# Kernel tuning notes

Measured on AMD Instinct MI355X. Metric: run time of the kernel, lower is better.

The kernel has to match this reference:

```python
import jax, jax.numpy as jnp
import numpy as np

# dims matching init_kwargs / input_specs
N, C, H, W = 8, 256, 64, 64
OUT_C, KH, KW = 256, 3, 3
STRIDE, PAD = 1, 1
OUT_H = (H - KH + 2 * PAD) // STRIDE + 1  # 64
OUT_W = (W - KW + 2 * PAD) // STRIDE + 1  # 64
K = KH * KW


def setup_inputs() -> dict:
    key = jax.random.key(0)
    k1, k2, k3 = jax.random.split(key, 3)
    x = jax.random.normal(k1, (N, C, H, W), dtype=jnp.float32)
    offset = jax.random.normal(k2, (N, 2 * K, OUT_H, OUT_W), dtype=jnp.float32)
    # kaiming-uniform-ish scale for weight (fan_in = C*KH*KW)
    bound = 1.0 / np.sqrt(C * KH * KW)
    weight = jax.random.uniform(k3, (OUT_C, C, KH, KW), dtype=jnp.float32,
                                minval=-bound, maxval=bound)
    return {"input": x, "offset": offset, "weight": weight}


def _deform_conv(x, offset, weight):
    # base sampling positions in pixel coords: y = oy*stride + ky - pad
    ky = jnp.repeat(jnp.arange(KH, dtype=jnp.float32) - PAD, KW)  # [K]
    kx = jnp.tile(jnp.arange(KW, dtype=jnp.float32) - PAD, KH)    # [K]
    oy = jnp.arange(OUT_H, dtype=jnp.float32) * STRIDE            # [outH]
    ox = jnp.arange(OUT_W, dtype=jnp.float32) * STRIDE            # [outW]
    base_y = ky[:, None, None] + oy[None, :, None]  # [K, outH, 1]
    base_x = kx[:, None, None] + ox[None, None, :]  # [K, 1, outW]

    off = offset.reshape(N, K, 2, OUT_H, OUT_W)
    y = base_y[None] + off[:, :, 0]  # [N, K, outH, outW], offset channel 0 = dy
    xp = base_x[None] + off[:, :, 1]  # channel 1 = dx

    # bilinear sample with zero padding (grid_sample align_corners=True, zeros)
    y0 = jnp.floor(y)
    x0 = jnp.floor(xp)
    bidx = jnp.arange(N)[:, None, None, None]
    acc = jnp.zeros((N, K, OUT_H, OUT_W, C), dtype=x.dtype)
    for dy in (0.0, 1.0):
        for dx in (0.0, 1.0):
            yi = y0 + dy
            xi = x0 + dx
            wgt = (1.0 - jnp.abs(y - yi)) * (1.0 - jnp.abs(xp - xi))
            valid = ((yi >= 0) & (yi <= H - 1) & (xi >= 0) & (xi <= W - 1))
            yc = jnp.clip(yi, 0, H - 1).astype(jnp.int32)
            xc = jnp.clip(xi, 0, W - 1).astype(jnp.int32)
            g = x[bidx, :, yc, xc]  # [N, K, outH, outW, C]
            acc = acc + g * (wgt * valid.astype(x.dtype))[..., None]

    # weight.view(outC, -1) flattens (C, KH, KW) -> (C, K) ordering
    w = weight.reshape(OUT_C, C, K)
    out = jnp.einsum('nkhwc,ock->nohw', acc, w)  # [N, outC, outH, outW]
    return out


def reference(input, offset, weight):
    # NOTE: original forward never adds bias -> faithfully omitted
    return _deform_conv(input, offset, weight)
```

## Files before the change

kernel.cpp:

```cpp
#include <hip/hip_runtime.h>
#include <hip/hip_fp16.h>
#include <stdint.h>


typedef _Float16 half8 __attribute__((ext_vector_type(8)));
typedef float f32x4 __attribute__((ext_vector_type(4)));

__device__ __forceinline__ __half2 h2(uint32_t u) {
  return __builtin_bit_cast(__half2, u);
}
__device__ __forceinline__ uint32_t packh2f(float a, float b) {
  return __builtin_bit_cast(uint32_t, __floats2half2_rn(a, b));
}
__device__ __forceinline__ __half2 duplo(uint32_t u) {
  return __half2half2(__builtin_bit_cast(__half, (unsigned short)(u & 0xffffu)));
}
__device__ __forceinline__ __half2 duphi(uint32_t u) {
  return __half2half2(__builtin_bit_cast(__half, (unsigned short)(u >> 16)));
}

__global__ __launch_bounds__(256) void prep_all_kernel(
    const float* __restrict__ x, const float* __restrict__ w,
    const float* __restrict__ offset,
    unsigned short* __restrict__ xb, unsigned short* __restrict__ w3s,
    unsigned short* __restrict__ coords) {
  __shared__ float tile[64][65];
  int tid = threadIdx.x;
  if (blockIdx.x < 2048) {
    int bn   = blockIdx.x >> 8;
    int rem  = blockIdx.x & 255;
    int y    = rem >> 2;
    int cblk = rem & 3;
    const float* src = x + ((size_t)(bn * 256 + cblk * 64)) * 4096 + y * 64;
#pragma unroll
    for (int i = 0; i < 4; ++i) {
      int u  = i * 256 + tid;
      int cl = u >> 4;
      int xs = (u & 15) * 4;
      float4 v = *(const float4*)(src + cl * 4096 + xs);
      tile[cl][xs] = v.x; tile[cl][xs + 1] = v.y;
      tile[cl][xs + 2] = v.z; tile[cl][xs + 3] = v.w;
    }
    __syncthreads();
    unsigned short* dst = xb + ((size_t)(bn * 64 + y) * 64) * 256 + cblk * 64;
#pragma unroll
    for (int i = 0; i < 8; ++i) {
      int v2  = i * 256 + tid;
      int xc  = v2 >> 5;
      int cl2 = (v2 & 31) * 2;
      *(uint32_t*)(dst + xc * 256 + cl2) = packh2f(tile[cl2][xc], tile[cl2 + 1][xc]);
    }
  } else if (blockIdx.x < 4352) {
    int idx = (blockIdx.x - 2048) * 256 + tid;
    int t    = idx >> 14;
    int r2   = idx & 16383;
    int e    = r2 & 7;
    int lane = (r2 >> 3) & 63;
    int ks   = (r2 >> 9) & 1;
    int nn   = (r2 >> 10) & 3;
    int wcol = (r2 >> 12) & 3;
    int oc = wcol * 64 + nn * 16 + (lane & 15);
    int kk = (ks * 4 + (lane >> 4)) * 8 + e;
    int c  = (t & 3) * 64 + kk;
    int k  = t >> 2;
    w3s[idx] = __builtin_bit_cast(unsigned short, __float2half(w[(oc * 256 + c) * 9 + k]));
  } else {
    int idx = (blockIdx.x - 4352) * 256 + tid;
    int ow  = idx & 63;
    int oh  = (idx >> 6) & 63;
    int r   = idx >> 12;
    int k   = r % 9;
    int bn  = r / 9;
    int ky = k / 3 - 1;
    int kx = k % 3 - 1;
    float offy = offset[((bn * 18 + 2 * k    ) * 64 + oh) * 64 + ow];
    float offx = offset[((bn * 18 + 2 * k + 1) * 64 + oh) * 64 + ow];
    float y = (float)(oh + ky) + offy;
    float x2 = (float)(ow + kx) + offx;
    float y0f = floorf(y), x0f = floorf(x2);
    float fy = y - y0f, fx = x2 - x0f;
    int y0 = (int)y0f, x0 = (int)x0f;
    int y1 = y0 + 1, x1 = x0 + 1;
    float vy0 = (y0 >= 0 && y0 <= 63) ? 1.0f : 0.0f;
    float vy1 = (y1 >= 0 && y1 <= 63) ? 1.0f : 0.0f;
    float vx0 = (x0 >= 0 && x0 <= 63) ? 1.0f : 0.0f;
    float vx1 = (x1 >= 0 && x1 <= 63) ? 1.0f : 0.0f;
    float wy0 = (1.0f - fy) * vy0, wy1 = fy * vy1;
    float wx0 = (1.0f - fx) * vx0, wx1 = fx * vx1;
    int y0c = min(max(y0, 0), 63), y1c = min(max(y1, 0), 63);
    int x0c = min(max(x0, 0), 63), x1c = min(max(x1, 0), 63);
    unsigned short ent[8];
    ent[0] = __builtin_bit_cast(unsigned short, __float2half(wy0 * wx0));
    ent[1] = __builtin_bit_cast(unsigned short, __float2half(wy0 * wx1));
    ent[2] = __builtin_bit_cast(unsigned short, __float2half(wy1 * wx0));
    ent[3] = __builtin_bit_cast(unsigned short, __float2half(wy1 * wx1));
    ent[4] = (unsigned short)(y0c * 64 + x0c);
    ent[5] = (unsigned short)(y0c * 64 + x1c);
    ent[6] = (unsigned short)(y1c * 64 + x0c);
    ent[7] = (unsigned short)(y1c * 64 + x1c);
    *(uint4*)(coords + (size_t)idx * 8) = *(const uint4*)ent;
  }
}

__global__ __launch_bounds__(512, 4) void deform_mfma_kernel(
    const unsigned short* __restrict__ xb,
    const unsigned short* __restrict__ coords,
    const unsigned short* __restrict__ w3s,
    float* __restrict__ out) {
  __shared__ __align__(16) unsigned short At[2][64 * 64];
  __shared__ __align__(16) unsigned short Bt[2][16384];

  int bn  = blockIdx.x & 7;
  int oh  = blockIdx.x >> 3;
  int tid = threadIdx.x;

  int w    = tid >> 6;
  int lane = tid & 63;
  int wrow = w & 1;
  int wcol = w >> 1;
  int mrow = lane & 15;
  int quad = lane >> 4;

  int srow = tid >> 3;
  int sg   = tid & 7;

  const char* xbc = (const char*)(xb + (size_t)bn * (64 * 64 * 256));
  const unsigned short* cb = coords + ((size_t)((bn * 9) * 64 + oh) * 64 + srow) * 8;

  int aw0  = srow * 64 + ((sg ^ (srow & 7)) * 8);
  int grp0 = quad ^ (mrow & 7);
  int grp1 = (4 + quad) ^ (mrow & 7);
  int a_base = (wrow * 32 + mrow) * 64;
  int b_off  = wcol * 4096 + lane * 8;
  int d_off  = w * 2048 + lane * 8;

  f32x4 acc[2][4] = {};

  __half2 w00, w01, w02, w03;
  uint32_t o00, o01, o02, o03;
  uint4 cn;
  uint4 ga0, ga1, ga2, ga3;

#define EBAR()                                                                  \
  {                                                                             \
    asm volatile("s_waitcnt vmcnt(0) lgkmcnt(0)" ::: "memory");                 \
    __builtin_amdgcn_sched_barrier(0);                                          \
    __builtin_amdgcn_s_barrier();                                               \
    asm volatile("" ::: "memory");                                              \
  }
#define CBAR()                                                                  \
  {                                                                             \
    asm volatile("s_waitcnt lgkmcnt(0)" ::: "memory");                          \
    __builtin_amdgcn_s_barrier();                                               \
    asm volatile("" ::: "memory");                                              \
  }
#define VMW(N)                                                                  \
  {                                                                             \
    asm volatile("s_waitcnt vmcnt(" #N ")" ::: "memory");                       \
    __builtin_amdgcn_sched_barrier(0);                                          \
  }

#define BDMA(TT, BB)                                                            \
  {                                                                             \
    const unsigned short* src = w3s + (size_t)(TT) * 16384 + d_off;             \
    unsigned short* dst = &Bt[BB][0] + w * 2048;                                \
    _Pragma("unroll")                                                           \
    for (int j = 0; j < 4; ++j) {                                               \
      __builtin_amdgcn_global_load_lds(                                         \
          (const __attribute__((address_space(1))) void*)(src + j * 512),       \
          (__attribute__((address_space(3))) void*)(dst + j * 512),             \
          16, 0, 0);                                                            \
    }                                                                           \
  }

#define TAPSETUP_R(CE)                                                          \
  {                                                                             \
    w00 = duplo((CE).x); w01 = duphi((CE).x);                                   \
    w02 = duplo((CE).y); w03 = duphi((CE).y);                                   \
    o00 = (((CE).z & 0xffffu) << 9) + sg * 16;                                  \
    o01 = (((CE).z >> 16) << 9) + sg * 16;                                      \
    o02 = (((CE).w & 0xffffu) << 9) + sg * 16;                                  \
    o03 = (((CE).w >> 16) << 9) + sg * 16;                                      \
  }

#define AGATHER(TT)                                                             \
  {                                                                             \
    ga0 = *(const uint4*)(xbc + o00 + ((TT) & 3) * 128);                        \
    ga1 = *(const uint4*)(xbc + o01 + ((TT) & 3) * 128);                        \
    ga2 = *(const uint4*)(xbc + o02 + ((TT) & 3) * 128);                        \
    ga3 = *(const uint4*)(xbc + o03 + ((TT) & 3) * 128);                        \
  }

#define AMATH(ATP)                                                              \
  {                                                                             \
    VMW(4)                                                                      \
    __half2 r0 = __hmul2(h2(ga0.x), w00);                                       \
    r0 = __hfma2(h2(ga1.x), w01, r0); r0 = __hfma2(h2(ga2.x), w02, r0);         \
    r0 = __hfma2(h2(ga3.x), w03, r0);                                           \
    __half2 r1 = __hmul2(h2(ga0.y), w00);                                       \
    r1 = __hfma2(h2(ga1.y), w01, r1); r1 = __hfma2(h2(ga2.y), w02, r1);         \
    r1 = __hfma2(h2(ga3.y), w03, r1);                                           \
    __half2 r2 = __hmul2(h2(ga0.z), w00);                                       \
    r2 = __hfma2(h2(ga1.z), w01, r2); r2 = __hfma2(h2(ga2.z), w02, r2);         \
    r2 = __hfma2(h2(ga3.z), w03, r2);                                           \
    __half2 r3 = __hmul2(h2(ga0.w), w00);                                       \
    r3 = __hfma2(h2(ga1.w), w01, r3); r3 = __hfma2(h2(ga2.w), w02, r3);         \
    r3 = __hfma2(h2(ga3.w), w03, r3);                                           \
    uint4 pk;                                                                   \
    pk.x = __builtin_bit_cast(uint32_t, r0);                                    \
    pk.y = __builtin_bit_cast(uint32_t, r1);                                    \
    pk.z = __builtin_bit_cast(uint32_t, r2);                                    \
    pk.w = __builtin_bit_cast(uint32_t, r3);                                    \
    *(uint4*)((ATP) + aw0) = pk;                                                \
  }

#define COMPUTE(ATP, BTP)                                                       \
  {                                                                             \
    half8 bfr[2][4];                                                            \
    _Pragma("unroll")                                                           \
    for (int nn = 0; nn < 4; ++nn) {                                            \
      bfr[0][nn] = *(const half8*)((BTP) + b_off + (nn * 2 + 0) * 512);         \
      bfr[1][nn] = *(const half8*)((BTP) + b_off + (nn * 2 + 1) * 512);         \
    }                                                                           \
    __builtin_amdgcn_s_setprio(1);                                              \
    _Pragma("unroll")                                                           \
    for (int m = 0; m < 2; ++m) {                                               \
      half8 af0 = *(const half8*)((ATP) + a_base + m * 1024 + grp0 * 8);        \
      half8 af1 = *(const half8*)((ATP) + a_base + m * 1024 + grp1 * 8);        \
      _Pragma("unroll")                                                         \
      for (int nn = 0; nn < 4; ++nn) {                                          \
        acc[m][nn] = __builtin_amdgcn_mfma_f32_16x16x32_f16(af0, bfr[0][nn], acc[m][nn], 0, 0, 0); \
        acc[m][nn] = __builtin_amdgcn_mfma_f32_16x16x32_f16(af1, bfr[1][nn], acc[m][nn], 0, 0, 0); \
      }                                                                         \
    }                                                                           \
    __builtin_amdgcn_s_setprio(0);                                              \
  }

  {
    uint4 ce0 = *(const uint4*)cb;
    AGATHER(0)
    TAPSETUP_R(ce0)
  }
  AGATHER(0)
  BDMA(0, 0)
  AMATH(&At[0][0])
  CBAR()

  for (int tap = 0; tap < 9; ++tap) {
#pragma unroll
    for (int cc = 0; cc < 4; ++cc) {
      const int t = tap * 4 + cc;
      EBAR()
      if (t < 35) {
        if (cc == 3) TAPSETUP_R(cn)
        if (cc == 2 && tap < 8) cn = *(const uint4*)(cb + (tap + 1) * 32768);
        AGATHER(t + 1)
        if (cc & 1) { BDMA(t + 1, 0) } else { BDMA(t + 1, 1) }
      }
      if (cc & 1) { COMPUTE(&At[1][0], &Bt[1][0]) } else { COMPUTE(&At[0][0], &Bt[0][0]) }
      if (t < 35) {
        if (cc & 1) { AMATH(&At[0][0]) } else { AMATH(&At[1][0]) }
      }
      CBAR()
    }
  }

  float* outp = out + (size_t)bn * 256 * 4096 + (size_t)oh * 64;
#pragma unroll
  for (int m = 0; m < 2; ++m) {
    int ow0 = wrow * 32 + m * 16 + quad * 4;
#pragma unroll
    for (int nn = 0; nn < 4; ++nn) {
      int oc = wcol * 64 + nn * 16 + mrow;
      *(f32x4*)(outp + (size_t)oc * 4096 + ow0) = acc[m][nn];
    }
  }
#undef EBAR
#undef CBAR
#undef VMW
#undef BDMA
#undef TAPSETUP_R
#undef AGATHER
#undef AMATH
#undef COMPUTE
}

extern "C" void kernel_launch(void* const* d_in, const int* in_sizes, int n_in,
                              void* d_out, int out_size, void* d_ws, size_t ws_size,
                              hipStream_t stream) {
  (void)in_sizes; (void)n_in; (void)out_size; (void)ws_size;
  const float* x      = (const float*)d_in[0];
  const float* offset = (const float*)d_in[1];
  const float* weight = (const float*)d_in[2];
  float* out = (float*)d_out;

  unsigned short* xb     = (unsigned short*)d_ws;
  unsigned short* w3s    = xb + (size_t)8 * 64 * 64 * 256;
  unsigned short* coords = w3s + (size_t)36 * 16384;

  prep_all_kernel<<<5504, 256, 0, stream>>>(x, weight, offset, xb, w3s, coords);
  deform_mfma_kernel<<<512, 512, 0, stream>>>(xb, coords, w3s, out);
}
```

Before: 144.1 us.

## Halve block to four waves, each computing 64x64 output tile

The MFMA kernel now runs 256 threads (4 waves) per block instead of 512. Each wave covers all 64 output columns for its 64 output channels, so the per-wave accumulator grows from 2x4 to 4x4 tiles. Each thread gathers and bilinearly blends two 16-byte chunks per tap and issues twice the weight DMA. The vmcnt waits are adjusted to match the larger number of outstanding loads. The aim is more MFMA work per A/B fragment load and less barrier cost per unit of work, at the price of more registers per thread, lower occupancy, and fewer waves available to hide gather latency.

```diff
diff --git a/kernel.cpp b/kernel.cpp
--- a/kernel.cpp
+++ b/kernel.cpp
@@ -102,7 +102,7 @@
   }
 }
 
-__global__ __launch_bounds__(512, 4) void deform_mfma_kernel(
+__global__ __launch_bounds__(256, 2) void deform_mfma_kernel(
     const unsigned short* __restrict__ xb,
     const unsigned short* __restrict__ coords,
     const unsigned short* __restrict__ w3s,
@@ -116,30 +116,29 @@
 
   int w    = tid >> 6;
   int lane = tid & 63;
-  int wrow = w & 1;
-  int wcol = w >> 1;
   int mrow = lane & 15;
   int quad = lane >> 4;
 
-  int srow = tid >> 3;
-  int sg   = tid & 7;
+  int srow = tid >> 2;
+  int sgl  = tid & 3;
 
   const char* xbc = (const char*)(xb + (size_t)bn * (64 * 64 * 256));
   const unsigned short* cb = coords + ((size_t)((bn * 9) * 64 + oh) * 64 + srow) * 8;
 
-  int aw0  = srow * 64 + ((sg ^ (srow & 7)) * 8);
+  int aw0  = srow * 64 + ((sgl ^ (srow & 7)) * 8);
+  int aw1  = srow * 64 + (((sgl + 4) ^ (srow & 7)) * 8);
   int grp0 = quad ^ (mrow & 7);
   int grp1 = (4 + quad) ^ (mrow & 7);
-  int a_base = (wrow * 32 + mrow) * 64;
-  int b_off  = wcol * 4096 + lane * 8;
-  int d_off  = w * 2048 + lane * 8;
-
-  f32x4 acc[2][4] = {};
+  int a_row = mrow * 64;
+  int b_off = w * 4096 + lane * 8;
+
+  f32x4 acc[4][4] = {};
 
   __half2 w00, w01, w02, w03;
   uint32_t o00, o01, o02, o03;
   uint4 cn;
   uint4 ga0, ga1, ga2, ga3;
+  uint4 gb0, gb1, gb2, gb3;
 
 #define EBAR()                                                                  \
   {                                                                             \
@@ -162,10 +161,10 @@
 
 #define BDMA(TT, BB)                                                            \
   {                                                                             \
-    const unsigned short* src = w3s + (size_t)(TT) * 16384 + d_off;             \
-    unsigned short* dst = &Bt[BB][0] + w * 2048;                                \
+    const unsigned short* src = w3s + (size_t)(TT) * 16384 + b_off;             \
+    unsigned short* dst = &Bt[BB][0] + b_off;                                   \
     _Pragma("unroll")                                                           \
-    for (int j = 0; j < 4; ++j) {                                               \
+    for (int j = 0; j < 8; ++j) {                                               \
       __builtin_amdgcn_global_load_lds(                                         \
           (const __attribute__((address_space(1))) void*)(src + j * 512),       \
           (__attribute__((address_space(3))) void*)(dst + j * 512),             \
@@ -177,10 +176,10 @@
   {                                                                             \
     w00 = duplo((CE).x); w01 = duphi((CE).x);                                   \
     w02 = duplo((CE).y); w03 = duphi((CE).y);                                   \
-    o00 = (((CE).z & 0xffffu) << 9) + sg * 16;                                  \
-    o01 = (((CE).z >> 16) << 9) + sg * 16;                                      \
-    o02 = (((CE).w & 0xffffu) << 9) + sg * 16;                                  \
-    o03 = (((CE).w >> 16) << 9) + sg * 16;                                      \
+    o00 = (((CE).z & 0xffffu) << 9) + sgl * 16;                                 \
+    o01 = (((CE).z >> 16) << 9) + sgl * 16;                                     \
+    o02 = (((CE).w & 0xffffu) << 9) + sgl * 16;                                 \
+    o03 = (((CE).w >> 16) << 9) + sgl * 16;                                     \
   }
 
 #define AGATHER(TT)                                                             \
@@ -189,11 +188,15 @@
     ga1 = *(const uint4*)(xbc + o01 + ((TT) & 3) * 128);                        \
     ga2 = *(const uint4*)(xbc + o02 + ((TT) & 3) * 128);                        \
     ga3 = *(const uint4*)(xbc + o03 + ((TT) & 3) * 128);                        \
-  }
-
-#define AMATH(ATP)                                                              \
-  {                                                                             \
-    VMW(4)                                                                      \
+    gb0 = *(const uint4*)(xbc + o00 + ((TT) & 3) * 128 + 64);                   \
+    gb1 = *(const uint4*)(xbc + o01 + ((TT) & 3) * 128 + 64);                   \
+    gb2 = *(const uint4*)(xbc + o02 + ((TT) & 3) * 128 + 64);                   \
+    gb3 = *(const uint4*)(xbc + o03 + ((TT) & 3) * 128 + 64);                   \
+  }
+
+#define AMATH(ATP, VM)                                                          \
+  {                                                                             \
+    VMW(VM)                                                                     \
     __half2 r0 = __hmul2(h2(ga0.x), w00);                                       \
     r0 = __hfma2(h2(ga1.x), w01, r0); r0 = __hfma2(h2(ga2.x), w02, r0);         \
     r0 = __hfma2(h2(ga3.x), w03, r0);                                           \
@@ -212,6 +215,24 @@
     pk.z = __builtin_bit_cast(uint32_t, r2);                                    \
     pk.w = __builtin_bit_cast(uint32_t, r3);                                    \
     *(uint4*)((ATP) + aw0) = pk;                                                \
+    __half2 s0 = __hmul2(h2(gb0.x), w00);                                       \
+    s0 = __hfma2(h2(gb1.x), w01, s0); s0 = __hfma2(h2(gb2.x), w02, s0);         \
+    s0 = __hfma2(h2(gb3.x), w03, s0);                                           \
+    __half2 s1 = __hmul2(h2(gb0.y), w00);                                       \
+    s1 = __hfma2(h2(gb1.y), w01, s1); s1 = __hfma2(h2(gb2.y), w02, s1);         \
+    s1 = __hfma2(h2(gb3.y), w03, s1);                                           \
+    __half2 s2 = __hmul2(h2(gb0.z), w00);                                       \
+    s2 = __hfma2(h2(gb1.z), w01, s2); s2 = __hfma2(h2(gb2.z), w02, s2);         \
+    s2 = __hfma2(h2(gb3.z), w03, s2);                                           \
+    __half2 s3 = __hmul2(h2(gb0.w), w00);                                       \
+    s3 = __hfma2(h2(gb1.w), w01, s3); s3 = __hfma2(h2(gb2.w), w02, s3);         \
+    s3 = __hfma2(h2(gb3.w), w03, s3);                                           \
+    uint4 qk;                                                                   \
+    qk.x = __builtin_bit_cast(uint32_t, s0);                                    \
+    qk.y = __builtin_bit_cast(uint32_t, s1);                                    \
+    qk.z = __builtin_bit_cast(uint32_t, s2);                                    \
+    qk.w = __builtin_bit_cast(uint32_t, s3);                                    \
+    *(uint4*)((ATP) + aw1) = qk;                                                \
   }
 
 #define COMPUTE(ATP, BTP)                                                       \
@@ -224,9 +245,9 @@
     }                                                                           \
     __builtin_amdgcn_s_setprio(1);                                              \
     _Pragma("unroll")                                                           \
-    for (int m = 0; m < 2; ++m) {                                               \
-      half8 af0 = *(const half8*)((ATP) + a_base + m * 1024 + grp0 * 8);        \
-      half8 af1 = *(const half8*)((ATP) + a_base + m * 1024 + grp1 * 8);        \
+    for (int m = 0; m < 4; ++m) {                                               \
+      half8 af0 = *(const half8*)((ATP) + m * 1024 + a_row + grp0 * 8);         \
+      half8 af1 = *(const half8*)((ATP) + m * 1024 + a_row + grp1 * 8);         \
       _Pragma("unroll")                                                         \
       for (int nn = 0; nn < 4; ++nn) {                                          \
         acc[m][nn] = __builtin_amdgcn_mfma_f32_16x16x32_f16(af0, bfr[0][nn], acc[m][nn], 0, 0, 0); \
@@ -238,12 +259,11 @@
 
   {
     uint4 ce0 = *(const uint4*)cb;
-    AGATHER(0)
     TAPSETUP_R(ce0)
   }
   AGATHER(0)
   BDMA(0, 0)
-  AMATH(&At[0][0])
+  AMATH(&At[0][0], 8)
   CBAR()
 
   for (int tap = 0; tap < 9; ++tap) {
@@ -253,13 +273,19 @@
       EBAR()
       if (t < 35) {
         if (cc == 3) TAPSETUP_R(cn)
+        AGATHER(t + 1)
         if (cc == 2 && tap < 8) cn = *(const uint4*)(cb + (tap + 1) * 32768);
-        AGATHER(t + 1)
         if (cc & 1) { BDMA(t + 1, 0) } else { BDMA(t + 1, 1) }
       }
       if (cc & 1) { COMPUTE(&At[1][0], &Bt[1][0]) } else { COMPUTE(&At[0][0], &Bt[0][0]) }
       if (t < 35) {
-        if (cc & 1) { AMATH(&At[0][0]) } else { AMATH(&At[1][0]) }
+        if (cc & 1) {
+          AMATH(&At[0][0], 8)
+        } else if (cc == 2 && tap < 8) {
+          AMATH(&At[1][0], 9)
+        } else {
+          AMATH(&At[1][0], 8)
+        }
       }
       CBAR()
     }
@@ -267,11 +293,11 @@
 
   float* outp = out + (size_t)bn * 256 * 4096 + (size_t)oh * 64;
 #pragma unroll
-  for (int m = 0; m < 2; ++m) {
-    int ow0 = wrow * 32 + m * 16 + quad * 4;
+  for (int m = 0; m < 4; ++m) {
+    int ow0 = m * 16 + quad * 4;
 #pragma unroll
     for (int nn = 0; nn < 4; ++nn) {
-      int oc = wcol * 64 + nn * 16 + mrow;
+      int oc = w * 64 + nn * 16 + mrow;
       *(f32x4*)(outp + (size_t)oc * 4096 + ow0) = acc[m][nn];
     }
   }
@@ -299,5 +325,5 @@
   unsigned short* coords = w3s + (size_t)36 * 16384;
 
   prep_all_kernel<<<5504, 256, 0, stream>>>(x, weight, offset, xb, w3s, coords);
-  deform_mfma_kernel<<<512, 512, 0, stream>>>(xb, coords, w3s, out);
-}
+  deform_mfma_kernel<<<512, 256, 0, stream>>>(xb, coords, w3s, out);
+}
```

New measurement: 150.3 us. 4.3% more time.
